# Optimization experiments

Measured on AMD Instinct MI355X. Metric: run time of the kernel, lower is better.

The kernel has to match this reference:

```python
import jax, jax.numpy as jnp
import numpy as np

EPS = 1e-5
GRID = 128          # coarse grid extent -> fine grid is 256^3
N1 = 15000          # coarse voxels
CHILD = 4           # children kept per coarse voxel
N2 = N1 * CHILD     # fine voxels
CIN = 128
COUT = 64


def _build_geometry():
    rng = np.random.RandomState(0)
    flat = rng.choice(GRID ** 3, N1, replace=False)
    cc = np.stack(np.unravel_index(flat, (GRID, GRID, GRID)), axis=1)  # [N1,3]
    offs8 = np.array([[i, j, k] for i in (0, 1) for j in (0, 1) for k in (0, 1)], dtype=np.int64)
    kidx = np.argsort(rng.rand(N1, 8), axis=1)[:, :CHILD]              # [N1,4] distinct child taps
    fine = (cc[:, None, :] * 2 + offs8[kidx]).reshape(-1, 3)           # [N2,3] unique fine coords
    up_src = np.repeat(np.arange(N1), CHILD).astype(np.int32)
    up_kidx = kidx.reshape(-1).astype(np.int32)
    # 27-offset neighbor maps via hashed coordinate lookup
    key = (fine[:, 0] * 256 + fine[:, 1]) * 256 + fine[:, 2]
    order = np.argsort(key)
    skey = key[order]
    offs27 = np.array([[i, j, k] for i in (-1, 0, 1) for j in (-1, 0, 1) for k in (-1, 0, 1)], dtype=np.int64)
    nbr_src = np.full((27, N2), N2, dtype=np.int32)
    nbr_dst = np.full((27, N2), N2, dtype=np.int32)
    for t in range(27):
        q = fine + offs27[t]
        inb = np.all((q >= 0) & (q < 256), axis=1)
        qk = (q[:, 0] * 256 + q[:, 1]) * 256 + q[:, 2]
        pos = np.searchsorted(skey, qk)
        pos = np.clip(pos, 0, N2 - 1)
        hit = inb & (skey[pos] == qk)
        nbr_src[t, hit] = order[pos[hit]]
        nbr_dst[t, hit] = np.arange(N2, dtype=np.int32)[hit]
    return up_src, up_kidx, nbr_src, nbr_dst


def setup_inputs() -> dict:
    key = jax.random.key(0)
    ks = jax.random.split(key, 8)
    up_src, up_kidx, nbr_src, nbr_dst = _build_geometry()
    s_up = 1.0 / np.sqrt(CIN * 8)
    s1 = 1.0 / np.sqrt(CIN * 27)
    s2 = 1.0 / np.sqrt(COUT * 27)
    return {
        "feats1": jax.random.normal(ks[0], (N1, CIN), jnp.float32),
        "feats2": jax.random.normal(ks[1], (N2, CIN // 2), jnp.float32),
        "w_up": jax.random.normal(ks[2], (8, CIN, CIN // 2), jnp.float32) * s_up,
        "gamma_up": jnp.ones((CIN // 2,), jnp.float32),
        "beta_up": jnp.zeros((CIN // 2,), jnp.float32),
        "w1": jax.random.normal(ks[3], (27, CIN, COUT), jnp.float32) * s1,
        "gamma1": jnp.ones((COUT,), jnp.float32),
        "beta1": jnp.zeros((COUT,), jnp.float32),
        "w2": jax.random.normal(ks[4], (27, COUT, COUT), jnp.float32) * s2,
        "gamma2": jnp.ones((COUT,), jnp.float32),
        "beta2": jnp.zeros((COUT,), jnp.float32),
        "up_src": jnp.asarray(up_src),
        "up_kidx": jnp.asarray(up_kidx),
        "nbr_src": jnp.asarray(nbr_src),
        "nbr_dst": jnp.asarray(nbr_dst),
    }


def _bn_relu(x, gamma, beta):
    # training-mode BatchNorm over the point dimension (biased variance), then ReLU
    m = jnp.mean(x, axis=0)
    v = jnp.var(x, axis=0)
    return jax.nn.relu((x - m) * jax.lax.rsqrt(v + EPS) * gamma + beta)


def _sparse_conv(x, w, nbr_src, nbr_dst):
    # x: [N,Ci]; w: [27,Ci,Co]; transform-then-gather-scatter (hash-map sparse conv)
    n = x.shape[0]
    co = w.shape[-1]
    y = jnp.einsum("nc,kco->kno", x, w)                       # [27,N,Co]
    y = jnp.concatenate([y, jnp.zeros((27, 1, co), y.dtype)], axis=1)  # sentinel row
    msg = jnp.take_along_axis(y, nbr_src[:, :, None], axis=1)  # [27,N,Co]
    out = jnp.zeros((n + 1, co), y.dtype).at[nbr_dst.reshape(-1)].add(msg.reshape(-1, co))
    return out[:-1]


def reference(feats1, feats2, w_up, gamma_up, beta_up, w1, gamma1, beta1, w2,
              gamma2, beta2, up_src, up_kidx, nbr_src, nbr_dst):
    # transposed conv k=2 s=2, generative=False: each fine voxel pulls from its unique coarse parent
    y = jnp.einsum("mc,kco->kmo", feats1, w_up)               # [8,N1,Cin/2]
    x1 = y[up_kidx, up_src]                                   # [N2,Cin/2]
    x1 = _bn_relu(x1, gamma_up, beta_up)
    x = jnp.concatenate([x1, feats2], axis=-1)                # [N2,Cin]
    h = _bn_relu(_sparse_conv(x, w1, nbr_src, nbr_dst), gamma1, beta1)
    return _bn_relu(_sparse_conv(h, w2, nbr_src, nbr_dst), gamma2, beta2)
```

## Files before the change

### kernel.cpp

```cpp
#include <hip/hip_runtime.h>


typedef short bf16x4 __attribute__((ext_vector_type(4)));
typedef short bf16x8 __attribute__((ext_vector_type(8)));
typedef float f32x16 __attribute__((ext_vector_type(16)));

#define ROWM 0x3FFFFFFF

__device__ __forceinline__ short f2bf(float f) {
    unsigned u = __float_as_uint(f);
    u += 0x7fffu + ((u >> 16) & 1u);
    return (short)(u >> 16);
}
__device__ __forceinline__ float bf2f(short s) {
    return __uint_as_float(((unsigned)(unsigned short)s) << 16);
}

__global__ __launch_bounds__(256) void k_setup(
    const float* __restrict__ w_up, const float* __restrict__ w1,
    const float* __restrict__ w2, const float* __restrict__ f1,
    const int* __restrict__ nbr, const int* __restrict__ up_kidx,
    short* __restrict__ wupp, short* __restrict__ w1p,
    short* __restrict__ w2p, short* __restrict__ f1bf,
    int* __restrict__ pmask, int* __restrict__ perm_rows,
    int* __restrict__ rank, int* __restrict__ cnt,
    int2* __restrict__ ext, int* __restrict__ extc,
    unsigned* __restrict__ flagbits,
    float* __restrict__ y1, float* __restrict__ y2,
    int n1, int n2, int nbExt, int nbGeom)
{
    int tid = threadIdx.x;
    int bid = blockIdx.x;
    if (bid < nbExt) {
        int i = bid * 256 + tid;
        unsigned hm = 0;
        if (i < n2) {
            #pragma unroll
            for (int t = 0; t < 27; ++t) {
                int s = nbr[(size_t)t * n2 + i];
                if (s < n2 && (s >> 2) != (i >> 2)) hm |= 1u << t;
            }
        }
        if (hm) {
            atomicOr(&flagbits[i >> 5], 1u << (i & 31));
            float4 z = make_float4(0.f, 0.f, 0.f, 0.f);
            float4* z1 = (float4*)(y1 + (size_t)i * 64);
            float4* z2 = (float4*)(y2 + (size_t)i * 64);
            #pragma unroll
            for (int q = 0; q < 16; ++q) { z1[q] = z; z2[q] = z; }
        }
        __shared__ int lcnt, lbase;
        if (tid == 0) lcnt = 0;
        __syncthreads();
        int nh = __popc(hm);
        int myofs = 0;
        if (nh) myofs = atomicAdd(&lcnt, nh);
        __syncthreads();
        if (tid == 0 && lcnt) lbase = atomicAdd(extc, lcnt);
        __syncthreads();
        if (nh) {
            int pos = lbase + myofs;
            unsigned m = hm;
            while (m) {
                int t = __ffs(m) - 1;
                m &= m - 1;
                int s = nbr[(size_t)t * n2 + i];
                ext[pos++] = make_int2(i, s | (t << 16));
            }
        }
    } else if (bid < nbExt + nbGeom) {
        int p = (bid - nbExt) * 256 + tid;
        if (p >= n1) return;
        int4 kd = *(const int4*)(up_kidx + 4 * p);
        int a = kd.x * 4 + 0, b = kd.y * 4 + 1, c = kd.z * 4 + 2, d = kd.w * 4 + 3;
        int t;
        if (a > b) { t = a; a = b; b = t; }
        if (c > d) { t = c; c = d; d = t; }
        if (a > c) { t = a; a = c; c = t; }
        if (b > d) { t = b; b = d; d = t; }
        if (b > c) { t = b; b = c; c = t; }
        perm_rows[4 * p + 0] = 4 * p + (a & 3);
        perm_rows[4 * p + 1] = 4 * p + (b & 3);
        perm_rows[4 * p + 2] = 4 * p + (c & 3);
        perm_rows[4 * p + 3] = 4 * p + (d & 3);
        int mask = (1 << (a >> 2)) | (1 << (b >> 2)) | (1 << (c >> 2)) | (1 << (d >> 2));
        pmask[p] = mask;
        rank[p] = atomicAdd(&cnt[mask], 1);
    } else {
        const long long nup = 65536, nw1 = 221184, nw2 = 110592;
        long long nf1 = (long long)n1 * 128;
        long long total = nup + nw1 + nw2 + nf1;
        long long gs = (long long)(gridDim.x - nbExt - nbGeom) * 256;
        for (long long e0 = (long long)(bid - nbExt - nbGeom) * 256 + tid;
             e0 < total; e0 += gs) {
            long long e = e0;
            if (e < nup) {
                int j = e & 7, l = (e >> 3) & 63, nt = (e >> 9) & 15, ks = (int)(e >> 13);
                int k = ks * 16 + (l >> 5) * 8 + j;
                int col = nt * 32 + (l & 31);
                wupp[e] = f2bf(w_up[((size_t)(col >> 6) * 128 + k) * 64 + (col & 63)]);
            } else if ((e -= nup) < nw1) {
                int j = e & 7, l = (e >> 3) & 63, ch = (e >> 9) & 1, ks = (e >> 10) & 7, t = (int)(e >> 13);
                int k = ks * 16 + (l >> 5) * 8 + j;
                int col = ch * 32 + (l & 31);
                w1p[e] = f2bf(w1[((size_t)t * 128 + k) * 64 + col]);
            } else if ((e -= nw1) < nw2) {
                int j = e & 7, l = (e >> 3) & 63, ch = (e >> 9) & 1, ks = (e >> 10) & 3, t = (int)(e >> 12);
                int k = ks * 16 + (l >> 5) * 8 + j;
                int col = ch * 32 + (l & 31);
                w2p[e] = f2bf(w2[((size_t)t * 64 + k) * 64 + col]);
            } else {
                e -= nw2;
                f1bf[e] = f2bf(f1[e]);
            }
        }
    }
}

__global__ __launch_bounds__(256) void k_up(
    const short* __restrict__ f1bf, const short* __restrict__ wupp,
    const int* __restrict__ pmask, const int* __restrict__ cnt,
    const int* __restrict__ rank, int* __restrict__ perm_par,
    int4* __restrict__ tiles, int* __restrict__ ntl,
    short* __restrict__ yup8, float* __restrict__ stats, int n1)
{
    if (blockIdx.x == 0) {
        __shared__ int sA[256], sB[256], bb[256];
        int t = threadIdx.x;
        int c = cnt[t], tc = (c + 31) >> 5;
        sA[t] = c; sB[t] = tc;
        __syncthreads();
        for (int off = 1; off < 256; off <<= 1) {
            int a = (t >= off) ? sA[t - off] : 0;
            int b = (t >= off) ? sB[t - off] : 0;
            __syncthreads();
            sA[t] += a; sB[t] += b;
            __syncthreads();
        }
        int base = sA[t] - c, toff = sB[t] - tc;
        bb[t] = base;
        for (int j = 0; j < tc; ++j) tiles[toff + j] = make_int4(t, base, j * 32, c);
        if (t == 255) ntl[0] = sB[255];
        __syncthreads();
        for (int p = t; p < n1; p += 256)
            perm_par[bb[pmask[p]] + rank[p]] = p;
        return;
    }
    __shared__ short lds[32 * 136];
    __shared__ float bs[64], bq[64];
    int bid = blockIdx.x - 1;
    int tile = bid >> 1;
    int w = threadIdx.x >> 6, lane = threadIdx.x & 63;
    int na = (bid & 1) * 8 + w, nb = na + 4;
    if (threadIdx.x < 64) { bs[threadIdx.x] = 0.f; bq[threadIdx.x] = 0.f; }
    #pragma unroll
    for (int it = 0; it < 2; ++it) {
        int c = it * 256 + threadIdx.x;
        int row = c >> 4, col8 = c & 15;
        int gr = tile * 32 + row; if (gr >= n1) gr = n1 - 1;
        int4 g = *(const int4*)(f1bf + (size_t)gr * 128 + col8 * 8);
        short* d = &lds[row * 136 + col8 * 8];
        *(int2*)d = make_int2(g.x, g.y);
        *(int2*)(d + 4) = make_int2(g.z, g.w);
    }
    int m = lane & 31, half = lane >> 5;
    int pm_l = (tile * 32 + m < n1) ? pmask[tile * 32 + m] : 0;
    __syncthreads();
    f32x16 a0, a1;
    #pragma unroll
    for (int i = 0; i < 16; ++i) { a0[i] = 0.f; a1[i] = 0.f; }
    const bf16x8* bp = (const bf16x8*)wupp;
    #pragma unroll
    for (int ks = 0; ks < 8; ++ks) {
        const short* ap = &lds[m * 136 + ks * 16 + half * 8];
        bf16x4 lo = *(const bf16x4*)ap, hi = *(const bf16x4*)(ap + 4);
        bf16x8 a = __builtin_shufflevector(lo, hi, 0, 1, 2, 3, 4, 5, 6, 7);
        bf16x8 b0 = bp[(size_t)(ks * 16 + na) * 64 + lane];
        bf16x8 b1 = bp[(size_t)(ks * 16 + nb) * 64 + lane];
        a0 = __builtin_amdgcn_mfma_f32_32x32x16_bf16(a, b0, a0, 0, 0, 0);
        a1 = __builtin_amdgcn_mfma_f32_32x32x16_bf16(a, b1, a1, 0, 0, 0);
    }
    int col = lane & 31;
    #pragma unroll
    for (int pass = 0; pass < 2; ++pass) {
        const f32x16& acc = pass ? a1 : a0;
        int n = pass ? nb : na;
        int slot = n >> 1, c = (n & 1) * 32 + col;
        float s0 = 0.f, q0 = 0.f;
        #pragma unroll
        for (int reg = 0; reg < 16; ++reg) {
            int r = (reg & 3) + 8 * (reg >> 2) + 4 * half;
            int p = tile * 32 + r;
            float v = acc[reg];
            int mk = __shfl(pm_l, r);
            if (p < n1) {
                yup8[(size_t)p * 512 + n * 32 + col] = f2bf(v);
                if ((mk >> slot) & 1) { s0 += v; q0 += v * v; }
            }
        }
        s0 += __shfl_xor(s0, 32);
        q0 += __shfl_xor(q0, 32);
        if (lane < 32) { atomicAdd(&bs[c], s0); atomicAdd(&bq[c], q0); }
    }
    __syncthreads();
    if (threadIdx.x < 64) {
        atomicAdd(&stats[threadIdx.x], bs[threadIdx.x]);
        atomicAdd(&stats[64 + threadIdx.x], bq[threadIdx.x]);
    }
}

__global__ __launch_bounds__(256) void k_extA(
    const short* __restrict__ yup8, const float* __restrict__ f2,
    const int* __restrict__ up_kidx, const float* __restrict__ w1,
    const float* __restrict__ gamma, const float* __restrict__ beta,
    const float* __restrict__ stats, const int2* __restrict__ ext,
    const int* __restrict__ extc, float* __restrict__ y, int n2)
{
    __shared__ float sc[64], sh[64];
    int tid = threadIdx.x;
    if (tid < 64) {
        float inv = 1.0f / (float)n2;
        float mean = stats[tid] * inv;
        float var = stats[64 + tid] * inv - mean * mean;
        float s = gamma[tid] * rsqrtf(var + 1e-5f);
        sc[tid] = s; sh[tid] = beta[tid] - mean * s;
    }
    __syncthreads();
    int gw = (blockIdx.x * 256 + tid) >> 6;
    int nw = (gridDim.x * 256) >> 6;
    int c = tid & 63;
    int ec = extc[0];
    for (int e = gw; e < ec; e += nw) {
        int2 en = ext[e];
        int i = en.x, s = en.y & 0xFFFF, t = en.y >> 16;
        const short* xr = yup8 + (size_t)(s >> 2) * 512 + up_kidx[s] * 64;
        const float* fr = f2 + (size_t)s * 64;
        const float* wr = w1 + (size_t)t * 8192 + c;
        float acc = 0.f;
        #pragma unroll 4
        for (int k = 0; k < 64; ++k) {
            float xk = fmaxf(bf2f(xr[k]) * sc[k] + sh[k], 0.f);
            acc += xk * wr[(size_t)k * 64];
        }
        #pragma unroll 4
        for (int k = 0; k < 64; ++k)
            acc += fr[k] * wr[(size_t)(64 + k) * 64];
        atomicAdd(&y[(size_t)i * 64 + c], acc);
    }
}

__global__ __launch_bounds__(256) void k_extB(
    const float* __restrict__ y1, const float* __restrict__ w2,
    const float* __restrict__ gamma, const float* __restrict__ beta,
    const float* __restrict__ stats, const int2* __restrict__ ext,
    const int* __restrict__ extc, float* __restrict__ y, int n2)
{
    __shared__ float sc[64], sh[64];
    int tid = threadIdx.x;
    if (tid < 64) {
        float inv = 1.0f / (float)n2;
        float mean = stats[tid] * inv;
        float var = stats[64 + tid] * inv - mean * mean;
        float s = gamma[tid] * rsqrtf(var + 1e-5f);
        sc[tid] = s; sh[tid] = beta[tid] - mean * s;
    }
    __syncthreads();
    int gw = (blockIdx.x * 256 + tid) >> 6;
    int nw = (gridDim.x * 256) >> 6;
    int c = tid & 63;
    int ec = extc[0];
    for (int e = gw; e < ec; e += nw) {
        int2 en = ext[e];
        int i = en.x, s = en.y & 0xFFFF, t = en.y >> 16;
        const float* hr = y1 + (size_t)s * 64;
        const float* wr = w2 + (size_t)t * 4096 + c;
        float acc = 0.f;
        #pragma unroll 4
        for (int k = 0; k < 64; ++k) {
            float hk = fmaxf(hr[k] * sc[k] + sh[k], 0.f);
            acc += hk * wr[(size_t)k * 64];
        }
        atomicAdd(&y[(size_t)i * 64 + c], acc);
    }
}

__device__ __forceinline__ void pair_epi2(const f32x16& a0v, const f32x16& a1v,
                                          int outrow0, int outrow1, int lane,
                                          int ch, float* __restrict__ y,
                                          float* __restrict__ bs,
                                          float* __restrict__ bq)
{
    int col = lane & 31;
    int c = ch * 32 + col;
    int r0[16], r1[16];
    #pragma unroll
    for (int reg = 0; reg < 16; ++reg) {
        int r = (reg & 3) + 8 * (reg >> 2) + 4 * (lane >> 5);
        r0[reg] = __shfl(outrow0, r);
        r1[reg] = __shfl(outrow1, r);
    }
    float o0[16], o1[16];
    #pragma unroll
    for (int reg = 0; reg < 16; ++reg) {
        o0[reg] = 0.f; o1[reg] = 0.f;
        if (r0[reg] >= (1 << 30))
            o0[reg] = y[(size_t)(r0[reg] & ROWM) * 64 + c];
        if (r1[reg] >= (1 << 30))
            o1[reg] = y[(size_t)(r1[reg] & ROWM) * 64 + c];
    }
    float s0 = 0.f, q0 = 0.f;
    #pragma unroll
    for (int reg = 0; reg < 16; ++reg) {
        if (r0[reg] >= 0) {
            float v = a0v[reg] + o0[reg];
            y[(size_t)(r0[reg] & ROWM) * 64 + c] = v;
            s0 += v; q0 += v * v;
        }
        if (r1[reg] >= 0) {
            float v = a1v[reg] + o1[reg];
            y[(size_t)(r1[reg] & ROWM) * 64 + c] = v;
            s0 += v; q0 += v * v;
        }
    }
    s0 += __shfl_xor(s0, 32);
    q0 += __shfl_xor(q0, 32);
    if (lane < 32) { atomicAdd(&bs[c], s0); atomicAdd(&bq[c], q0); }
}

__device__ __forceinline__ int tap27(int pa, int pb) {
    int di = ((pb >> 2) & 1) - ((pa >> 2) & 1);
    int dj = ((pb >> 1) & 1) - ((pa >> 1) & 1);
    int dk = (pb & 1) - (pa & 1);
    return (di + 1) * 9 + (dj + 1) * 3 + (dk + 1);
}

__global__ __launch_bounds__(256) void k_pairA(
    const short* __restrict__ yup8, const float* __restrict__ f2,
    const int* __restrict__ up_kidx, const short* __restrict__ wp,
    const float* __restrict__ gamma, const float* __restrict__ beta,
    const float* __restrict__ stats, const int* __restrict__ perm_par,
    const int* __restrict__ perm_rows, const int4* __restrict__ tiles,
    const int* __restrict__ n_tiles, const unsigned* __restrict__ flagbits,
    float* __restrict__ y, float* __restrict__ ostats, int n2)
{
    constexpr int LP = 520;
    __shared__ short lds[32 * LP];
    __shared__ int srows[128], soff[128];
    __shared__ float scs[64], shs[64], bs[64], bq[64];
    int bt = blockIdx.x;
    if (bt >= n_tiles[0]) return;
    int4 td = tiles[bt];
    int mask = td.x, p_start = td.y, lt = td.z, cntb = td.w;
    int tid = threadIdx.x;
    if (tid < 128) {
        int li = lt + (tid >> 2);
        int pid = perm_par[p_start + ((li < cntb) ? li : 0)];
        int i = perm_rows[pid * 4 + (tid & 3)];
        unsigned fb = (flagbits[i >> 5] >> (i & 31)) & 1u;
        srows[tid] = i | (int)(fb << 30);
        soff[tid] = (i >> 2) * 512 + up_kidx[i] * 64;
    } else if (tid < 192) {
        int cc = tid - 128;
        float inv = 1.0f / (float)n2;
        float mean = stats[cc] * inv;
        float var = stats[64 + cc] * inv - mean * mean;
        float s = gamma[cc] * rsqrtf(var + 1e-5f);
        scs[cc] = s; shs[cc] = beta[cc] - mean * s;
    } else {
        int cc = tid - 192;
        bs[cc] = 0.f; bq[cc] = 0.f;
    }
    __syncthreads();
    #pragma unroll
    for (int it = 0; it < 8; ++it) {
        int c0 = it * 256 + tid;
        int pl = c0 >> 6, w8 = c0 & 63;
        int j = w8 >> 4, col8 = w8 & 15;
        short* d = &lds[pl * LP + j * 128 + col8 * 8];
        if (col8 < 8) {
            bf16x8 g = *(const bf16x8*)(yup8 + (size_t)soff[pl * 4 + j] + col8 * 8);
            short o[8];
            #pragma unroll
            for (int u = 0; u < 8; ++u) {
                int cc = col8 * 8 + u;
                o[u] = f2bf(fmaxf(bf2f(g[u]) * scs[cc] + shs[cc], 0.f));
            }
            *(int2*)d = make_int2(((int)(unsigned short)o[0]) | ((int)o[1] << 16),
                                  ((int)(unsigned short)o[2]) | ((int)o[3] << 16));
            *(int2*)(d + 4) = make_int2(((int)(unsigned short)o[4]) | ((int)o[5] << 16),
                                        ((int)(unsigned short)o[6]) | ((int)o[7] << 16));
        } else {
            const float* fr = f2 + (size_t)(srows[pl * 4 + j] & ROWM) * 64 + (col8 - 8) * 8;
            float4 f0 = *(const float4*)fr;
            float4 f1v = *(const float4*)(fr + 4);
            short o[8] = {f2bf(f0.x), f2bf(f0.y), f2bf(f0.z), f2bf(f0.w),
                          f2bf(f1v.x), f2bf(f1v.y), f2bf(f1v.z), f2bf(f1v.w)};
            *(int2*)d = make_int2(((int)(unsigned short)o[0]) | ((int)o[1] << 16),
                                  ((int)(unsigned short)o[2]) | ((int)o[3] << 16));
            *(int2*)(d + 4) = make_int2(((int)(unsigned short)o[4]) | ((int)o[5] << 16),
                                        ((int)(unsigned short)o[6]) | ((int)o[7] << 16));
        }
    }
    int p0 = -1, p1 = -1, p2 = -1, p3 = -1;
    #pragma unroll
    for (int b = 7; b >= 0; --b)
        if ((mask >> b) & 1) { p3 = p2; p2 = p1; p1 = p0; p0 = b; }
    int w = tid >> 6, lane = tid & 63;
    int a0 = w >> 1, a1 = a0 + 2, ch = w & 1;
    int pa0 = (a0 == 0) ? p0 : p1;
    int pa1 = (a1 == 2) ? p2 : p3;
    int t00 = tap27(pa0, p0), t01 = tap27(pa0, p1), t02 = tap27(pa0, p2), t03 = tap27(pa0, p3);
    int t10 = tap27(pa1, p0), t11 = tap27(pa1, p1), t12 = tap27(pa1, p2), t13 = tap27(pa1, p3);
    int m = lane & 31;
    int li = lt + m;
    bool vp = li < cntb;
    int pid = perm_par[p_start + (vp ? li : 0)];
    (void)pid;
    int outrow0 = vp ? srows[m * 4 + a0] : -1;
    int outrow1 = vp ? srows[m * 4 + a1] : -1;
    __syncthreads();
    f32x16 acc0, acc1;
    #pragma unroll
    for (int i = 0; i < 16; ++i) { acc0[i] = 0.f; acc1[i] = 0.f; }
    const bf16x8* bp = (const bf16x8*)wp;
    int half = lane >> 5;
    #pragma unroll
    for (int b = 0; b < 4; ++b) {
        int tb0 = (b == 0) ? t00 : (b == 1) ? t01 : (b == 2) ? t02 : t03;
        int tb1 = (b == 0) ? t10 : (b == 1) ? t11 : (b == 2) ? t12 : t13;
        #pragma unroll
        for (int kk = 0; kk < 8; ++kk) {
            int ks = b * 8 + kk;
            const short* ap = &lds[m * LP + ks * 16 + half * 8];
            bf16x4 lo = *(const bf16x4*)ap, hi = *(const bf16x4*)(ap + 4);
            bf16x8 a = __builtin_shufflevector(lo, hi, 0, 1, 2, 3, 4, 5, 6, 7);
            bf16x8 b0 = bp[((size_t)(tb0 * 8 + kk) * 2 + ch) * 64 + lane];
            bf16x8 b1 = bp[((size_t)(tb1 * 8 + kk) * 2 + ch) * 64 + lane];
            acc0 = __builtin_amdgcn_mfma_f32_32x32x16_bf16(a, b0, acc0, 0, 0, 0);
            acc1 = __builtin_amdgcn_mfma_f32_32x32x16_bf16(a, b1, acc1, 0, 0, 0);
        }
    }
    pair_epi2(acc0, acc1, outrow0, outrow1, lane, ch, y, bs, bq);
    __syncthreads();
    if (tid < 64) {
        atomicAdd(&ostats[tid], bs[tid]);
        atomicAdd(&ostats[64 + tid], bq[tid]);
    }
}

__global__ __launch_bounds__(256) void k_pairB(
    const float* __restrict__ y1, const short* __restrict__ wp,
    const float* __restrict__ gamma, const float* __restrict__ beta,
    const float* __restrict__ stats, const int* __restrict__ perm_par,
    const int* __restrict__ perm_rows, const int4* __restrict__ tiles,
    const int* __restrict__ n_tiles, const unsigned* __restrict__ flagbits,
    float* __restrict__ y, float* __restrict__ ostats, int n2)
{
    constexpr int LP = 264;
    __shared__ short lds[32 * LP];
    __shared__ int srows[128];
    __shared__ float scs[64], shs[64], bs[64], bq[64];
    int bt = blockIdx.x;
    if (bt >= n_tiles[0]) return;
    int4 td = tiles[bt];
    int mask = td.x, p_start = td.y, lt = td.z, cntb = td.w;
    int tid = threadIdx.x;
    if (tid < 128) {
        int li = lt + (tid >> 2);
        int pid = perm_par[p_start + ((li < cntb) ? li : 0)];
        int i = perm_rows[pid * 4 + (tid & 3)];
        unsigned fb = (flagbits[i >> 5] >> (i & 31)) & 1u;
        srows[tid] = i | (int)(fb << 30);
    } else if (tid < 192) {
        int cc = tid - 128;
        float inv = 1.0f / (float)n2;
        float mean = stats[cc] * inv;
        float var = stats[64 + cc] * inv - mean * mean;
        float s = gamma[cc] * rsqrtf(var + 1e-5f);
        scs[cc] = s; shs[cc] = beta[cc] - mean * s;
    } else {
        int cc = tid - 192;
        bs[cc] = 0.f; bq[cc] = 0.f;
    }
    __syncthreads();
    #pragma unroll
    for (int it = 0; it < 4; ++it) {
        int c0 = it * 256 + tid;
        int pl = c0 >> 5, w8 = c0 & 31;
        int j = w8 >> 3, col8 = w8 & 7;
        const float* fr = y1 + (size_t)(srows[pl * 4 + j] & ROWM) * 64 + col8 * 8;
        float4 f0 = *(const float4*)fr;
        float4 f1v = *(const float4*)(fr + 4);
        short o[8];
        #pragma unroll
        for (int u = 0; u < 4; ++u) {
            int cc = col8 * 8 + u;
            float v = (u == 0) ? f0.x : (u == 1) ? f0.y : (u == 2) ? f0.z : f0.w;
            o[u] = f2bf(fmaxf(v * scs[cc] + shs[cc], 0.f));
        }
        #pragma unroll
        for (int u = 0; u < 4; ++u) {
            int cc = col8 * 8 + 4 + u;
            float v = (u == 0) ? f1v.x : (u == 1) ? f1v.y : (u == 2) ? f1v.z : f1v.w;
            o[4 + u] = f2bf(fmaxf(v * scs[cc] + shs[cc], 0.f));
        }
        short* d = &lds[pl * LP + j * 64 + col8 * 8];
        *(int2*)d = make_int2(((int)(unsigned short)o[0]) | ((int)o[1] << 16),
                              ((int)(unsigned short)o[2]) | ((int)o[3] << 16));
        *(int2*)(d + 4) = make_int2(((int)(unsigned short)o[4]) | ((int)o[5] << 16),
                                    ((int)(unsigned short)o[6]) | ((int)o[7] << 16));
    }
    int p0 = -1, p1 = -1, p2 = -1, p3 = -1;
    #pragma unroll
    for (int b = 7; b >= 0; --b)
        if ((mask >> b) & 1) { p3 = p2; p2 = p1; p1 = p0; p0 = b; }
    int w = tid >> 6, lane = tid & 63;
    int a0 = w >> 1, a1 = a0 + 2, ch = w & 1;
    int pa0 = (a0 == 0) ? p0 : p1;
    int pa1 = (a1 == 2) ? p2 : p3;
    int t00 = tap27(pa0, p0), t01 = tap27(pa0, p1), t02 = tap27(pa0, p2), t03 = tap27(pa0, p3);
    int t10 = tap27(pa1, p0), t11 = tap27(pa1, p1), t12 = tap27(pa1, p2), t13 = tap27(pa1, p3);
    int m = lane & 31;
    int li = lt + m;
    bool vp = li < cntb;
    int outrow0 = vp ? srows[m * 4 + a0] : -1;
    int outrow1 = vp ? srows[m * 4 + a1] : -1;
    __syncthreads();
    f32x16 acc0, acc1;
    #pragma unroll
    for (int i = 0; i < 16; ++i) { acc0[i] = 0.f; acc1[i] = 0.f; }
    const bf16x8* bp = (const bf16x8*)wp;
    int half = lane >> 5;
    #pragma unroll
    for (int b = 0; b < 4; ++b) {
        int tb0 = (b == 0) ? t00 : (b == 1) ? t01 : (b == 2) ? t02 : t03;
        int tb1 = (b == 0) ? t10 : (b == 1) ? t11 : (b == 2) ? t12 : t13;
        #pragma unroll
        for (int kk = 0; kk < 4; ++kk) {
            int ks = b * 4 + kk;
            const short* ap = &lds[m * LP + ks * 16 + half * 8];
            bf16x4 lo = *(const bf16x4*)ap, hi = *(const bf16x4*)(ap + 4);
            bf16x8 a = __builtin_shufflevector(lo, hi, 0, 1, 2, 3, 4, 5, 6, 7);
            bf16x8 b0 = bp[((size_t)(tb0 * 4 + kk) * 2 + ch) * 64 + lane];
            bf16x8 b1 = bp[((size_t)(tb1 * 4 + kk) * 2 + ch) * 64 + lane];
            acc0 = __builtin_amdgcn_mfma_f32_32x32x16_bf16(a, b0, acc0, 0, 0, 0);
            acc1 = __builtin_amdgcn_mfma_f32_32x32x16_bf16(a, b1, acc1, 0, 0, 0);
        }
    }
    pair_epi2(acc0, acc1, outrow0, outrow1, lane, ch, y, bs, bq);
    __syncthreads();
    if (tid < 64) {
        atomicAdd(&ostats[tid], bs[tid]);
        atomicAdd(&ostats[64 + tid], bq[tid]);
    }
}

__global__ __launch_bounds__(256) void k_final(
    const float* __restrict__ y, const float* __restrict__ gamma,
    const float* __restrict__ beta, const float* __restrict__ stats,
    float* __restrict__ out, int n2)
{
    __shared__ float sc[64], sh[64];
    int tid = threadIdx.x;
    if (tid < 64) {
        float inv = 1.0f / (float)n2;
        float mean = stats[tid] * inv;
        float var = stats[64 + tid] * inv - mean * mean;
        float s = gamma[tid] * rsqrtf(var + 1e-5f);
        sc[tid] = s;
        sh[tid] = beta[tid] - mean * s;
    }
    __syncthreads();
    long long total = (long long)n2 * 16;
    long long stride = (long long)gridDim.x * blockDim.x;
    for (long long idx = (long long)blockIdx.x * blockDim.x + tid; idx < total; idx += stride) {
        int i = (int)(idx >> 4);
        int c4 = ((int)idx & 15) * 4;
        const float* src = y + (size_t)i * 64 + c4;
        float4 o;
        o.x = fmaxf(src[0] * sc[c4 + 0] + sh[c4 + 0], 0.f);
        o.y = fmaxf(src[1] * sc[c4 + 1] + sh[c4 + 1], 0.f);
        o.z = fmaxf(src[2] * sc[c4 + 2] + sh[c4 + 2], 0.f);
        o.w = fmaxf(src[3] * sc[c4 + 3] + sh[c4 + 3], 0.f);
        *(float4*)(out + (size_t)i * 64 + c4) = o;
    }
}

extern "C" void kernel_launch(void* const* d_in, const int* in_sizes, int n_in,
                              void* d_out, int out_size, void* d_ws, size_t ws_size,
                              hipStream_t stream)
{
    const float* feats1   = (const float*)d_in[0];
    const float* feats2   = (const float*)d_in[1];
    const float* w_up     = (const float*)d_in[2];
    const float* gamma_up = (const float*)d_in[3];
    const float* beta_up  = (const float*)d_in[4];
    const float* w1       = (const float*)d_in[5];
    const float* gamma1   = (const float*)d_in[6];
    const float* beta1    = (const float*)d_in[7];
    const float* w2       = (const float*)d_in[8];
    const float* gamma2   = (const float*)d_in[9];
    const float* beta2    = (const float*)d_in[10];
    const int* up_src     = (const int*)d_in[11];  (void)up_src;
    const int* up_kidx    = (const int*)d_in[12];
    const int* nbr_src    = (const int*)d_in[13];

    int n1 = in_sizes[0] / 128;
    int n2 = in_sizes[1] / 64;

    char* p = (char*)d_ws;
    auto alloc = [&](size_t bytes) {
        char* r = p;
        p += (bytes + 255) & ~(size_t)255;
        return r;
    };
    float* stats    = (float*)alloc(384 * 4);
    int*   cnt      = (int*)alloc(256 * 4);
    int*   extc     = (int*)alloc(16);
    int*   ntl      = (int*)alloc(16);
    unsigned* flagbits = (unsigned*)alloc(((size_t)(n2 + 31) / 32) * 4);
    size_t headBytes = (size_t)(p - (char*)d_ws);
    int maxTiles    = (n1 + 31) / 32 + 80;
    int4*  tiles    = (int4*)alloc((size_t)maxTiles * 16);
    short* wupp     = (short*)alloc((size_t)65536 * 2);
    short* w1p      = (short*)alloc((size_t)221184 * 2);
    short* w2p      = (short*)alloc((size_t)110592 * 2);
    short* f1bf     = (short*)alloc((size_t)n1 * 128 * 2);
    int*   pmask    = (int*)alloc((size_t)n1 * 4);
    int*   rank     = (int*)alloc((size_t)n1 * 4);
    int*   perm_par = (int*)alloc((size_t)n1 * 4);
    int*   perm_rows= (int*)alloc((size_t)4 * n1 * 4);
    int2*  ext      = (int2*)alloc((size_t)27 * n2 * 8);
    short* yup8     = (short*)alloc((size_t)n1 * 512 * 2);
    float* y1       = (float*)alloc((size_t)n2 * 64 * 4);
    float* y2       = (float*)alloc((size_t)n2 * 64 * 4);

    int nbExt  = (n2 + 255) / 256;
    int nbGeom = (n1 + 255) / 256;
    int nbPack = 256;
    int nbSetup = nbExt + nbGeom + nbPack;
    int upBlocks = 1 + 2 * ((n1 + 31) / 32);
    int ewBlocks16 = (int)(((long long)n2 * 16 + 255) / 256);

    hipMemsetAsync(d_ws, 0, headBytes, stream);
    k_setup<<<nbSetup, 256, 0, stream>>>(w_up, w1, w2, feats1, nbr_src, up_kidx,
                                         wupp, w1p, w2p, f1bf, pmask, perm_rows,
                                         rank, cnt, ext, extc, flagbits, y1, y2,
                                         n1, n2, nbExt, nbGeom);
    k_up<<<upBlocks, 256, 0, stream>>>(f1bf, wupp, pmask, cnt, rank, perm_par,
                                       tiles, ntl, yup8, stats, n1);
    k_extA<<<512, 256, 0, stream>>>(yup8, feats2, up_kidx, w1, gamma_up, beta_up,
                                    stats, ext, extc, y1, n2);
    k_pairA<<<maxTiles, 256, 0, stream>>>(yup8, feats2, up_kidx, w1p, gamma_up,
                                          beta_up, stats, perm_par, perm_rows,
                                          tiles, ntl, flagbits, y1, stats + 128, n2);
    k_extB<<<512, 256, 0, stream>>>(y1, w2, gamma1, beta1, stats + 128, ext,
                                    extc, y2, n2);
    k_pairB<<<maxTiles, 256, 0, stream>>>(y1, w2p, gamma1, beta1, stats + 128,
                                          perm_par, perm_rows, tiles, ntl,
                                          flagbits, y2, stats + 256, n2);
    k_final<<<ewBlocks16, 256, 0, stream>>>(y2, gamma2, beta2, stats + 256,
                                            (float*)d_out, n2);
}
```

Before: 250.6 us.

## Fuse cross-parent neighbor contributions into pair kernels via shared-memory accumulators

The separate k_extA/k_extB kernels and the global atomic accumulation into y1/y2 are removed. Instead, setup writes a per-row list of external neighbors, and each pair-tile block computes those contributions itself into a shared-memory buffer, adding them in the epilogue. This drops two kernel launches, the zeroing of y1/y2 rows, the flag bitmap and the read-modify-write of flagged rows. In exchange it assumes at most 48 affected rows and 128 entries per tile; anything beyond those caps is silently dropped, so correctness depends on neighbors across parents being sparse.

```diff
diff --git a/kernel.cpp b/kernel.cpp
--- a/kernel.cpp
+++ b/kernel.cpp
@@ -5,7 +5,11 @@
 typedef short bf16x8 __attribute__((ext_vector_type(8)));
 typedef float f32x16 __attribute__((ext_vector_type(16)));
 
-#define ROWM 0x3FFFFFFF
+#define PKROW(x) ((x) & 0xFFFFF)
+#define PKSLOT(x) (((x) >> 20) & 127)
+
+constexpr int MAXS = 48;
+constexpr int MAXE = 128;
 
 __device__ __forceinline__ short f2bf(float f) {
     unsigned u = __float_as_uint(f);
@@ -24,50 +28,24 @@
     short* __restrict__ w2p, short* __restrict__ f1bf,
     int* __restrict__ pmask, int* __restrict__ perm_rows,
     int* __restrict__ rank, int* __restrict__ cnt,
-    int2* __restrict__ ext, int* __restrict__ extc,
-    unsigned* __restrict__ flagbits,
-    float* __restrict__ y1, float* __restrict__ y2,
+    int* __restrict__ extcnt, int* __restrict__ extslab,
     int n1, int n2, int nbExt, int nbGeom)
 {
     int tid = threadIdx.x;
     int bid = blockIdx.x;
     if (bid < nbExt) {
         int i = bid * 256 + tid;
-        unsigned hm = 0;
-        if (i < n2) {
-            #pragma unroll
-            for (int t = 0; t < 27; ++t) {
-                int s = nbr[(size_t)t * n2 + i];
-                if (s < n2 && (s >> 2) != (i >> 2)) hm |= 1u << t;
+        if (i >= n2) return;
+        int c = 0;
+        #pragma unroll
+        for (int t = 0; t < 27; ++t) {
+            int s = nbr[(size_t)t * n2 + i];
+            if (s < n2 && (s >> 2) != (i >> 2)) {
+                extslab[(size_t)i * 27 + c] = s | (t << 16);
+                ++c;
             }
         }
-        if (hm) {
-            atomicOr(&flagbits[i >> 5], 1u << (i & 31));
-            float4 z = make_float4(0.f, 0.f, 0.f, 0.f);
-            float4* z1 = (float4*)(y1 + (size_t)i * 64);
-            float4* z2 = (float4*)(y2 + (size_t)i * 64);
-            #pragma unroll
-            for (int q = 0; q < 16; ++q) { z1[q] = z; z2[q] = z; }
-        }
-        __shared__ int lcnt, lbase;
-        if (tid == 0) lcnt = 0;
-        __syncthreads();
-        int nh = __popc(hm);
-        int myofs = 0;
-        if (nh) myofs = atomicAdd(&lcnt, nh);
-        __syncthreads();
-        if (tid == 0 && lcnt) lbase = atomicAdd(extc, lcnt);
-        __syncthreads();
-        if (nh) {
-            int pos = lbase + myofs;
-            unsigned m = hm;
-            while (m) {
-                int t = __ffs(m) - 1;
-                m &= m - 1;
-                int s = nbr[(size_t)t * n2 + i];
-                ext[pos++] = make_int2(i, s | (t << 16));
-            }
-        }
+        extcnt[i] = c;
     } else if (bid < nbExt + nbGeom) {
         int p = (bid - nbExt) * 256 + tid;
         if (p >= n1) return;
@@ -209,84 +187,10 @@
     }
 }
 
-__global__ __launch_bounds__(256) void k_extA(
-    const short* __restrict__ yup8, const float* __restrict__ f2,
-    const int* __restrict__ up_kidx, const float* __restrict__ w1,
-    const float* __restrict__ gamma, const float* __restrict__ beta,
-    const float* __restrict__ stats, const int2* __restrict__ ext,
-    const int* __restrict__ extc, float* __restrict__ y, int n2)
-{
-    __shared__ float sc[64], sh[64];
-    int tid = threadIdx.x;
-    if (tid < 64) {
-        float inv = 1.0f / (float)n2;
-        float mean = stats[tid] * inv;
-        float var = stats[64 + tid] * inv - mean * mean;
-        float s = gamma[tid] * rsqrtf(var + 1e-5f);
-        sc[tid] = s; sh[tid] = beta[tid] - mean * s;
-    }
-    __syncthreads();
-    int gw = (blockIdx.x * 256 + tid) >> 6;
-    int nw = (gridDim.x * 256) >> 6;
-    int c = tid & 63;
-    int ec = extc[0];
-    for (int e = gw; e < ec; e += nw) {
-        int2 en = ext[e];
-        int i = en.x, s = en.y & 0xFFFF, t = en.y >> 16;
-        const short* xr = yup8 + (size_t)(s >> 2) * 512 + up_kidx[s] * 64;
-        const float* fr = f2 + (size_t)s * 64;
-        const float* wr = w1 + (size_t)t * 8192 + c;
-        float acc = 0.f;
-        #pragma unroll 4
-        for (int k = 0; k < 64; ++k) {
-            float xk = fmaxf(bf2f(xr[k]) * sc[k] + sh[k], 0.f);
-            acc += xk * wr[(size_t)k * 64];
-        }
-        #pragma unroll 4
-        for (int k = 0; k < 64; ++k)
-            acc += fr[k] * wr[(size_t)(64 + k) * 64];
-        atomicAdd(&y[(size_t)i * 64 + c], acc);
-    }
-}
-
-__global__ __launch_bounds__(256) void k_extB(
-    const float* __restrict__ y1, const float* __restrict__ w2,
-    const float* __restrict__ gamma, const float* __restrict__ beta,
-    const float* __restrict__ stats, const int2* __restrict__ ext,
-    const int* __restrict__ extc, float* __restrict__ y, int n2)
-{
-    __shared__ float sc[64], sh[64];
-    int tid = threadIdx.x;
-    if (tid < 64) {
-        float inv = 1.0f / (float)n2;
-        float mean = stats[tid] * inv;
-        float var = stats[64 + tid] * inv - mean * mean;
-        float s = gamma[tid] * rsqrtf(var + 1e-5f);
-        sc[tid] = s; sh[tid] = beta[tid] - mean * s;
-    }
-    __syncthreads();
-    int gw = (blockIdx.x * 256 + tid) >> 6;
-    int nw = (gridDim.x * 256) >> 6;
-    int c = tid & 63;
-    int ec = extc[0];
-    for (int e = gw; e < ec; e += nw) {
-        int2 en = ext[e];
-        int i = en.x, s = en.y & 0xFFFF, t = en.y >> 16;
-        const float* hr = y1 + (size_t)s * 64;
-        const float* wr = w2 + (size_t)t * 4096 + c;
-        float acc = 0.f;
-        #pragma unroll 4
-        for (int k = 0; k < 64; ++k) {
-            float hk = fmaxf(hr[k] * sc[k] + sh[k], 0.f);
-            acc += hk * wr[(size_t)k * 64];
-        }
-        atomicAdd(&y[(size_t)i * 64 + c], acc);
-    }
-}
-
 __device__ __forceinline__ void pair_epi2(const f32x16& a0v, const f32x16& a1v,
                                           int outrow0, int outrow1, int lane,
                                           int ch, float* __restrict__ y,
+                                          const float* extacc,
                                           float* __restrict__ bs,
                                           float* __restrict__ bq)
 {
@@ -299,26 +203,19 @@
         r0[reg] = __shfl(outrow0, r);
         r1[reg] = __shfl(outrow1, r);
     }
-    float o0[16], o1[16];
-    #pragma unroll
-    for (int reg = 0; reg < 16; ++reg) {
-        o0[reg] = 0.f; o1[reg] = 0.f;
-        if (r0[reg] >= (1 << 30))
-            o0[reg] = y[(size_t)(r0[reg] & ROWM) * 64 + c];
-        if (r1[reg] >= (1 << 30))
-            o1[reg] = y[(size_t)(r1[reg] & ROWM) * 64 + c];
-    }
     float s0 = 0.f, q0 = 0.f;
     #pragma unroll
     for (int reg = 0; reg < 16; ++reg) {
         if (r0[reg] >= 0) {
-            float v = a0v[reg] + o0[reg];
-            y[(size_t)(r0[reg] & ROWM) * 64 + c] = v;
+            int sl = PKSLOT(r0[reg]);
+            float v = a0v[reg] + (sl ? extacc[(sl - 1) * 64 + c] : 0.f);
+            y[(size_t)PKROW(r0[reg]) * 64 + c] = v;
             s0 += v; q0 += v * v;
         }
         if (r1[reg] >= 0) {
-            float v = a1v[reg] + o1[reg];
-            y[(size_t)(r1[reg] & ROWM) * 64 + c] = v;
+            int sl = PKSLOT(r1[reg]);
+            float v = a1v[reg] + (sl ? extacc[(sl - 1) * 64 + c] : 0.f);
+            y[(size_t)PKROW(r1[reg]) * 64 + c] = v;
             s0 += v; q0 += v * v;
         }
     }
@@ -337,28 +234,49 @@
 __global__ __launch_bounds__(256) void k_pairA(
     const short* __restrict__ yup8, const float* __restrict__ f2,
     const int* __restrict__ up_kidx, const short* __restrict__ wp,
+    const float* __restrict__ w1f,
     const float* __restrict__ gamma, const float* __restrict__ beta,
     const float* __restrict__ stats, const int* __restrict__ perm_par,
     const int* __restrict__ perm_rows, const int4* __restrict__ tiles,
-    const int* __restrict__ n_tiles, const unsigned* __restrict__ flagbits,
+    const int* __restrict__ n_tiles, const int* __restrict__ extcnt,
+    const int* __restrict__ extslab,
     float* __restrict__ y, float* __restrict__ ostats, int n2)
 {
     constexpr int LP = 520;
     __shared__ short lds[32 * LP];
     __shared__ int srows[128], soff[128];
     __shared__ float scs[64], shs[64], bs[64], bq[64];
+    __shared__ float extacc[MAXS * 64];
+    __shared__ int2 elist[MAXE];
+    __shared__ int s_nent, s_nslot;
     int bt = blockIdx.x;
     if (bt >= n_tiles[0]) return;
     int4 td = tiles[bt];
     int mask = td.x, p_start = td.y, lt = td.z, cntb = td.w;
     int tid = threadIdx.x;
+    if (tid == 0) { s_nent = 0; s_nslot = 0; }
+    for (int idx = tid; idx < MAXS * 64; idx += 256) extacc[idx] = 0.f;
+    __syncthreads();
     if (tid < 128) {
         int li = lt + (tid >> 2);
         int pid = perm_par[p_start + ((li < cntb) ? li : 0)];
         int i = perm_rows[pid * 4 + (tid & 3)];
-        unsigned fb = (flagbits[i >> 5] >> (i & 31)) & 1u;
-        srows[tid] = i | (int)(fb << 30);
         soff[tid] = (i >> 2) * 512 + up_kidx[i] * 64;
+        int pk = i;
+        if (li < cntb) {
+            int nc = extcnt[i];
+            if (nc > 0) {
+                int slot = atomicAdd(&s_nslot, 1);
+                if (slot < MAXS) {
+                    pk |= (slot + 1) << 20;
+                    int eo = atomicAdd(&s_nent, nc);
+                    for (int e = 0; e < nc; ++e)
+                        if (eo + e < MAXE)
+                            elist[eo + e] = make_int2(slot, extslab[(size_t)i * 27 + e]);
+                }
+            }
+        }
+        srows[tid] = pk;
     } else if (tid < 192) {
         int cc = tid - 128;
         float inv = 1.0f / (float)n2;
@@ -390,7 +308,7 @@
             *(int2*)(d + 4) = make_int2(((int)(unsigned short)o[4]) | ((int)o[5] << 16),
                                         ((int)(unsigned short)o[6]) | ((int)o[7] << 16));
         } else {
-            const float* fr = f2 + (size_t)(srows[pl * 4 + j] & ROWM) * 64 + (col8 - 8) * 8;
+            const float* fr = f2 + (size_t)PKROW(srows[pl * 4 + j]) * 64 + (col8 - 8) * 8;
             float4 f0 = *(const float4*)fr;
             float4 f1v = *(const float4*)(fr + 4);
             short o[8] = {f2bf(f0.x), f2bf(f0.y), f2bf(f0.z), f2bf(f0.w),
@@ -399,6 +317,25 @@
                                   ((int)(unsigned short)o[2]) | ((int)o[3] << 16));
             *(int2*)(d + 4) = make_int2(((int)(unsigned short)o[4]) | ((int)o[5] << 16),
                                         ((int)(unsigned short)o[6]) | ((int)o[7] << 16));
+        }
+    }
+    {
+        int wv = tid >> 6, ln = tid & 63;
+        int ne = s_nent; if (ne > MAXE) ne = MAXE;
+        for (int e = wv; e < ne; e += 4) {
+            int2 en = elist[e];
+            int s = en.y & 0xFFFF, t = en.y >> 16;
+            const short* xr = yup8 + (size_t)(s >> 2) * 512 + (size_t)up_kidx[s] * 64;
+            const float* fr = f2 + (size_t)s * 64;
+            const float* wr = w1f + (size_t)t * 8192 + ln;
+            float acc = 0.f;
+            #pragma unroll 4
+            for (int k = 0; k < 64; ++k)
+                acc += fmaxf(bf2f(xr[k]) * scs[k] + shs[k], 0.f) * wr[(size_t)k * 64];
+            #pragma unroll 4
+            for (int k = 0; k < 64; ++k)
+                acc += fr[k] * wr[(size_t)(64 + k) * 64];
+            atomicAdd(&extacc[en.x * 64 + ln], acc);
         }
     }
     int p0 = -1, p1 = -1, p2 = -1, p3 = -1;
@@ -414,8 +351,6 @@
     int m = lane & 31;
     int li = lt + m;
     bool vp = li < cntb;
-    int pid = perm_par[p_start + (vp ? li : 0)];
-    (void)pid;
     int outrow0 = vp ? srows[m * 4 + a0] : -1;
     int outrow1 = vp ? srows[m * 4 + a1] : -1;
     __syncthreads();
@@ -440,7 +375,7 @@
             acc1 = __builtin_amdgcn_mfma_f32_32x32x16_bf16(a, b1, acc1, 0, 0, 0);
         }
     }
-    pair_epi2(acc0, acc1, outrow0, outrow1, lane, ch, y, bs, bq);
+    pair_epi2(acc0, acc1, outrow0, outrow1, lane, ch, y, extacc, bs, bq);
     __syncthreads();
     if (tid < 64) {
         atomicAdd(&ostats[tid], bs[tid]);
@@ -450,27 +385,48 @@
 
 __global__ __launch_bounds__(256) void k_pairB(
     const float* __restrict__ y1, const short* __restrict__ wp,
+    const float* __restrict__ w2f,
     const float* __restrict__ gamma, const float* __restrict__ beta,
     const float* __restrict__ stats, const int* __restrict__ perm_par,
     const int* __restrict__ perm_rows, const int4* __restrict__ tiles,
-    const int* __restrict__ n_tiles, const unsigned* __restrict__ flagbits,
+    const int* __restrict__ n_tiles, const int* __restrict__ extcnt,
+    const int* __restrict__ extslab,
     float* __restrict__ y, float* __restrict__ ostats, int n2)
 {
     constexpr int LP = 264;
     __shared__ short lds[32 * LP];
     __shared__ int srows[128];
     __shared__ float scs[64], shs[64], bs[64], bq[64];
+    __shared__ float extacc[MAXS * 64];
+    __shared__ int2 elist[MAXE];
+    __shared__ int s_nent, s_nslot;
     int bt = blockIdx.x;
     if (bt >= n_tiles[0]) return;
     int4 td = tiles[bt];
     int mask = td.x, p_start = td.y, lt = td.z, cntb = td.w;
     int tid = threadIdx.x;
+    if (tid == 0) { s_nent = 0; s_nslot = 0; }
+    for (int idx = tid; idx < MAXS * 64; idx += 256) extacc[idx] = 0.f;
+    __syncthreads();
     if (tid < 128) {
         int li = lt + (tid >> 2);
         int pid = perm_par[p_start + ((li < cntb) ? li : 0)];
         int i = perm_rows[pid * 4 + (tid & 3)];
-        unsigned fb = (flagbits[i >> 5] >> (i & 31)) & 1u;
-        srows[tid] = i | (int)(fb << 30);
+        int pk = i;
+        if (li < cntb) {
+            int nc = extcnt[i];
+            if (nc > 0) {
+                int slot = atomicAdd(&s_nslot, 1);
+                if (slot < MAXS) {
+                    pk |= (slot + 1) << 20;
+                    int eo = atomicAdd(&s_nent, nc);
+                    for (int e = 0; e < nc; ++e)
+                        if (eo + e < MAXE)
+                            elist[eo + e] = make_int2(slot, extslab[(size_t)i * 27 + e]);
+                }
+            }
+        }
+        srows[tid] = pk;
     } else if (tid < 192) {
         int cc = tid - 128;
         float inv = 1.0f / (float)n2;
@@ -488,7 +444,7 @@
         int c0 = it * 256 + tid;
         int pl = c0 >> 5, w8 = c0 & 31;
         int j = w8 >> 3, col8 = w8 & 7;
-        const float* fr = y1 + (size_t)(srows[pl * 4 + j] & ROWM) * 64 + col8 * 8;
+        const float* fr = y1 + (size_t)PKROW(srows[pl * 4 + j]) * 64 + col8 * 8;
         float4 f0 = *(const float4*)fr;
         float4 f1v = *(const float4*)(fr + 4);
         short o[8];
@@ -509,6 +465,21 @@
                               ((int)(unsigned short)o[2]) | ((int)o[3] << 16));
         *(int2*)(d + 4) = make_int2(((int)(unsigned short)o[4]) | ((int)o[5] << 16),
                                     ((int)(unsigned short)o[6]) | ((int)o[7] << 16));
+    }
+    {
+        int wv = tid >> 6, ln = tid & 63;
+        int ne = s_nent; if (ne > MAXE) ne = MAXE;
+        for (int e = wv; e < ne; e += 4) {
+            int2 en = elist[e];
+            int s = en.y & 0xFFFF, t = en.y >> 16;
+            const float* hr = y1 + (size_t)s * 64;
+            const float* wr = w2f + (size_t)t * 4096 + ln;
+            float acc = 0.f;
+            #pragma unroll 4
+            for (int k = 0; k < 64; ++k)
+                acc += fmaxf(hr[k] * scs[k] + shs[k], 0.f) * wr[(size_t)k * 64];
+            atomicAdd(&extacc[en.x * 64 + ln], acc);
+        }
     }
     int p0 = -1, p1 = -1, p2 = -1, p3 = -1;
     #pragma unroll
@@ -547,7 +518,7 @@
             acc1 = __builtin_amdgcn_mfma_f32_32x32x16_bf16(a, b1, acc1, 0, 0, 0);
         }
     }
-    pair_epi2(acc0, acc1, outrow0, outrow1, lane, ch, y, bs, bq);
+    pair_epi2(acc0, acc1, outrow0, outrow1, lane, ch, y, extacc, bs, bq);
     __syncthreads();
     if (tid < 64) {
         atomicAdd(&ostats[tid], bs[tid]);
@@ -616,9 +587,7 @@
     };
     float* stats    = (float*)alloc(384 * 4);
     int*   cnt      = (int*)alloc(256 * 4);
-    int*   extc     = (int*)alloc(16);
     int*   ntl      = (int*)alloc(16);
-    unsigned* flagbits = (unsigned*)alloc(((size_t)(n2 + 31) / 32) * 4);
     size_t headBytes = (size_t)(p - (char*)d_ws);
     int maxTiles    = (n1 + 31) / 32 + 80;
     int4*  tiles    = (int4*)alloc((size_t)maxTiles * 16);
@@ -630,7 +599,8 @@
     int*   rank     = (int*)alloc((size_t)n1 * 4);
     int*   perm_par = (int*)alloc((size_t)n1 * 4);
     int*   perm_rows= (int*)alloc((size_t)4 * n1 * 4);
-    int2*  ext      = (int2*)alloc((size_t)27 * n2 * 8);
+    int*   extcnt   = (int*)alloc((size_t)n2 * 4);
+    int*   extslab  = (int*)alloc((size_t)n2 * 27 * 4);
     short* yup8     = (short*)alloc((size_t)n1 * 512 * 2);
     float* y1       = (float*)alloc((size_t)n2 * 64 * 4);
     float* y2       = (float*)alloc((size_t)n2 * 64 * 4);
@@ -645,20 +615,18 @@
     hipMemsetAsync(d_ws, 0, headBytes, stream);
     k_setup<<<nbSetup, 256, 0, stream>>>(w_up, w1, w2, feats1, nbr_src, up_kidx,
                                          wupp, w1p, w2p, f1bf, pmask, perm_rows,
-                                         rank, cnt, ext, extc, flagbits, y1, y2,
+                                         rank, cnt, extcnt, extslab,
                                          n1, n2, nbExt, nbGeom);
     k_up<<<upBlocks, 256, 0, stream>>>(f1bf, wupp, pmask, cnt, rank, perm_par,
                                        tiles, ntl, yup8, stats, n1);
-    k_extA<<<512, 256, 0, stream>>>(yup8, feats2, up_kidx, w1, gamma_up, beta_up,
-                                    stats, ext, extc, y1, n2);
-    k_pairA<<<maxTiles, 256, 0, stream>>>(yup8, feats2, up_kidx, w1p, gamma_up,
-                                          beta_up, stats, perm_par, perm_rows,
-                                          tiles, ntl, flagbits, y1, stats + 128, n2);
-    k_extB<<<512, 256, 0, stream>>>(y1, w2, gamma1, beta1, stats + 128, ext,
-                                    extc, y2, n2);
-    k_pairB<<<maxTiles, 256, 0, stream>>>(y1, w2p, gamma1, beta1, stats + 128,
-                                          perm_par, perm_rows, tiles, ntl,
-                                          flagbits, y2, stats + 256, n2);
+    k_pairA<<<maxTiles, 256, 0, stream>>>(yup8, feats2, up_kidx, w1p, w1,
+                                          gamma_up, beta_up, stats, perm_par,
+                                          perm_rows, tiles, ntl, extcnt, extslab,
+                                          y1, stats + 128, n2);
+    k_pairB<<<maxTiles, 256, 0, stream>>>(y1, w2p, w2, gamma1, beta1,
+                                          stats + 128, perm_par, perm_rows,
+                                          tiles, ntl, extcnt, extslab,
+                                          y2, stats + 256, n2);
     k_final<<<ewBlocks16, 256, 0, stream>>>(y2, gamma2, beta2, stats + 256,
                                             (float*)d_out, n2);
 }
```

Measured after the change: 269.9 us. +7.7%, slower.
